# Kernel optimization log

Measured on AMD Instinct MI355X. Metric: run time of the kernel, lower is better.

Reference implementation:

```python
import jax, jax.numpy as jnp
import numpy as np

B, NQ, NK = 8, 1024, 1024
DQ = DK = DV = 512
H = 8
DH = DV // H
EPS = 1e-5
NEG = -1e9


def _layer_norm(x, g, b):
    mu = jnp.mean(x, axis=-1, keepdims=True)
    var = jnp.mean(jnp.square(x - mu), axis=-1, keepdims=True)
    return (x - mu) * jax.lax.rsqrt(var + EPS) * g + b


def setup_inputs() -> dict:
    key = jax.random.key(0)
    ks = jax.random.split(key, 16)
    s_q = 1.0 / np.sqrt(DQ)
    s_k = 1.0 / np.sqrt(DK)
    s_v = 1.0 / np.sqrt(DV)
    return {
        "Q": jax.random.normal(ks[0], (B, NQ, DQ), jnp.float32),
        "K": jax.random.normal(ks[1], (B, NK, DK), jnp.float32),
        "mask": jax.random.randint(ks[2], (B, NK), 0, 2, jnp.int32),
        "Wq": jax.random.uniform(ks[3], (DQ, DV), jnp.float32, -s_q, s_q),
        "bq": jax.random.uniform(ks[4], (DV,), jnp.float32, -s_q, s_q),
        "Wk": jax.random.uniform(ks[5], (DK, DV), jnp.float32, -s_k, s_k),
        "bk": jax.random.uniform(ks[6], (DV,), jnp.float32, -s_k, s_k),
        "Wv": jax.random.uniform(ks[7], (DK, DV), jnp.float32, -s_k, s_k),
        "bv": jax.random.uniform(ks[8], (DV,), jnp.float32, -s_k, s_k),
        "Wo": jax.random.uniform(ks[9], (DV, DV), jnp.float32, -s_v, s_v),
        "bo": jax.random.uniform(ks[10], (DV,), jnp.float32, -s_v, s_v),
        "g0": jnp.ones((DV,), jnp.float32),
        "b0": jnp.zeros((DV,), jnp.float32),
        "g1": jnp.ones((DV,), jnp.float32),
        "b1": jnp.zeros((DV,), jnp.float32),
    }


def reference(Q, K, mask, Wq, bq, Wk, bk, Wv, bv, Wo, bo, g0, b0, g1, b1):
    b = Q.shape[0]
    # projections: [B, N, DV] -> [B, N, H, DH]
    q = (Q @ Wq + bq).reshape(b, -1, H, DH)
    k = (K @ Wk + bk).reshape(b, -1, H, DH)
    v = (K @ Wv + bv).reshape(b, -1, H, DH)
    scores = jnp.einsum("bqhd,bkhd->bhqk", q, k) / np.sqrt(DH)  # [B,H,Nq,Nk]
    scores = jnp.where((mask == 0)[:, None, None, :], NEG, scores)
    A = jax.nn.softmax(scores, axis=-1)
    o = q + jnp.einsum("bhqk,bkhd->bqhd", A, v)  # residual on projected Q (per head)
    O = o.reshape(b, -1, DV)
    O = _layer_norm(O, g0, b0)
    O = O + jax.nn.relu(O @ Wo + bo)
    O = _layer_norm(O, g1, b1)
    return O
```

## Files before the change

kernel.cpp:

```cpp
#include <hip/hip_runtime.h>


typedef float f32x4 __attribute__((ext_vector_type(4)));
typedef short bf16x8 __attribute__((ext_vector_type(8)));
typedef unsigned short u16;

#define MFMA16 __builtin_amdgcn_mfma_f32_16x16x32_bf16

__device__ __forceinline__ float bf2f(u16 u){
    unsigned x = ((unsigned)u) << 16;
    return __builtin_bit_cast(float, x);
}
__device__ __forceinline__ u16 f2bf(float f){
    unsigned u = __builtin_bit_cast(unsigned, f);
    u = u + 0x7fffu + ((u >> 16) & 1u);
    return (u16)(u >> 16);
}

__global__ __launch_bounds__(256) void transpose_w(
    const float* __restrict__ Wq, const float* __restrict__ Wk,
    const float* __restrict__ Wv, const float* __restrict__ Wo,
    u16* __restrict__ wt)
{
    const int z = blockIdx.z;
    const float* W = (z == 0) ? Wq : (z == 1) ? Wk : (z == 2) ? Wv : Wo;
    u16* out = wt + (size_t)z * 512 * 512;

    __shared__ u16 tile[32][33];
    const int k0 = blockIdx.y * 32, n0 = blockIdx.x * 32;
    const int c = threadIdx.x & 31, r = threadIdx.x >> 5;
#pragma unroll
    for (int i = 0; i < 4; i++) {
        int rr = r + i * 8;
        tile[rr][c] = f2bf(W[(size_t)(k0 + rr) * 512 + n0 + c]);
    }
    __syncthreads();
#pragma unroll
    for (int i = 0; i < 4; i++) {
        int rr = r + i * 8;
        out[(size_t)(n0 + rr) * 512 + k0 + c] = tile[c][rr];
    }
}

__global__ __launch_bounds__(256) void transpose_v(
    const u16* __restrict__ vb, u16* __restrict__ vtg)
{
    __shared__ u16 tile[32][33];
    const int bh = blockIdx.z;
    const int b = bh >> 3, h = bh & 7;
    const int k0 = blockIdx.x * 32, d0 = blockIdx.y * 32;
    const int c = threadIdx.x & 31, r = threadIdx.x >> 5;
#pragma unroll
    for (int i = 0; i < 4; i++) {
        int rr = r + i * 8;
        tile[rr][c] = vb[(size_t)(b * 1024 + k0 + rr) * 512 + h * 64 + d0 + c];
    }
    __syncthreads();
#pragma unroll
    for (int i = 0; i < 4; i++) {
        int rr = r + i * 8;
        vtg[(size_t)(bh * 64 + d0 + rr) * 1024 + k0 + c] = tile[c][rr];
    }
}

__global__ __launch_bounds__(256) void gemm_proj(
    const float* __restrict__ Q, const float* __restrict__ K,
    const u16* __restrict__ wt,
    const float* __restrict__ bq, const float* __restrict__ bk, const float* __restrict__ bv,
    u16* __restrict__ qb, u16* __restrict__ kb, u16* __restrict__ vb)
{
    __shared__ __align__(16) u16 lds_a[128 * 40];
    __shared__ __align__(16) u16 lds_b[128 * 40];

    const int z = blockIdx.z;
    const float* X = (z == 0) ? Q : K;
    const u16* Wt = wt + (size_t)z * 512 * 512;
    const float* bias = (z == 0) ? bq : (z == 1) ? bk : bv;
    u16* outb = (z == 0) ? qb : (z == 1) ? kb : vb;

    const int bm = blockIdx.y, bn = blockIdx.x;
    const int t = threadIdx.x;
    const int wave = t >> 6, lane = t & 63, quad = lane >> 4, lm = lane & 15;
    const int wm = wave >> 1, wn = wave & 1;

    f32x4 acc[4][4];
    const f32x4 zz = {0.f, 0.f, 0.f, 0.f};
#pragma unroll
    for (int i = 0; i < 4; i++)
#pragma unroll
        for (int j = 0; j < 4; j++) acc[i][j] = zz;

    for (int k0 = 0; k0 < 512; k0 += 32) {
#pragma unroll
        for (int i = 0; i < 2; i++) {
            int idx = t + i * 256;
            int r = idx >> 2, c = (idx & 3) * 8;
            const float* xp = &X[(size_t)(bm * 128 + r) * 512 + k0 + c];
            f32x4 a0 = *(const f32x4*)xp;
            f32x4 a1 = *(const f32x4*)(xp + 4);
            bf16x8 xv;
#pragma unroll
            for (int j = 0; j < 4; j++) { xv[j] = (short)f2bf(a0[j]); xv[4 + j] = (short)f2bf(a1[j]); }
            *(bf16x8*)&lds_a[r * 40 + c] = xv;
            *(bf16x8*)&lds_b[r * 40 + c] =
                *(const bf16x8*)&Wt[(size_t)(bn * 128 + r) * 512 + k0 + c];
        }
        __syncthreads();
        bf16x8 af[4], bfr[4];
#pragma unroll
        for (int mi = 0; mi < 4; mi++)
            af[mi] = *(const bf16x8*)&lds_a[(wm * 64 + mi * 16 + lm) * 40 + quad * 8];
#pragma unroll
        for (int ni = 0; ni < 4; ni++)
            bfr[ni] = *(const bf16x8*)&lds_b[(wn * 64 + ni * 16 + lm) * 40 + quad * 8];
#pragma unroll
        for (int mi = 0; mi < 4; mi++)
#pragma unroll
            for (int ni = 0; ni < 4; ni++)
                acc[mi][ni] = MFMA16(af[mi], bfr[ni], acc[mi][ni], 0, 0, 0);
        __syncthreads();
    }

#pragma unroll
    for (int mi = 0; mi < 4; mi++) {
#pragma unroll
        for (int ni = 0; ni < 4; ni++) {
            const int col = bn * 128 + wn * 64 + ni * 16 + lm;
            const float bv_ = bias[col];
#pragma unroll
            for (int r = 0; r < 4; r++) {
                const int row = bm * 128 + wm * 64 + mi * 16 + quad * 4 + r;
                outb[(size_t)row * 512 + col] = f2bf(acc[mi][ni][r] + bv_);
            }
        }
    }
}

__global__ __launch_bounds__(256) void gemm_mlp(
    const u16* __restrict__ X, const u16* __restrict__ wt,
    const float* __restrict__ bo, const float* __restrict__ resid,
    float* __restrict__ outf)
{
    __shared__ __align__(16) u16 lds_a[128 * 40];
    __shared__ __align__(16) u16 lds_b[128 * 40];

    const u16* Wt = wt + (size_t)3 * 512 * 512;
    const int bm = blockIdx.y, bn = blockIdx.x;
    const int t = threadIdx.x;
    const int wave = t >> 6, lane = t & 63, quad = lane >> 4, lm = lane & 15;
    const int wm = wave >> 1, wn = wave & 1;

    f32x4 acc[4][4];
    const f32x4 zz = {0.f, 0.f, 0.f, 0.f};
#pragma unroll
    for (int i = 0; i < 4; i++)
#pragma unroll
        for (int j = 0; j < 4; j++) acc[i][j] = zz;

    for (int k0 = 0; k0 < 512; k0 += 32) {
#pragma unroll
        for (int i = 0; i < 2; i++) {
            int idx = t + i * 256;
            int r = idx >> 2, c = (idx & 3) * 8;
            *(bf16x8*)&lds_a[r * 40 + c] =
                *(const bf16x8*)&X[(size_t)(bm * 128 + r) * 512 + k0 + c];
            *(bf16x8*)&lds_b[r * 40 + c] =
                *(const bf16x8*)&Wt[(size_t)(bn * 128 + r) * 512 + k0 + c];
        }
        __syncthreads();
        bf16x8 af[4], bfr[4];
#pragma unroll
        for (int mi = 0; mi < 4; mi++)
            af[mi] = *(const bf16x8*)&lds_a[(wm * 64 + mi * 16 + lm) * 40 + quad * 8];
#pragma unroll
        for (int ni = 0; ni < 4; ni++)
            bfr[ni] = *(const bf16x8*)&lds_b[(wn * 64 + ni * 16 + lm) * 40 + quad * 8];
#pragma unroll
        for (int mi = 0; mi < 4; mi++)
#pragma unroll
            for (int ni = 0; ni < 4; ni++)
                acc[mi][ni] = MFMA16(af[mi], bfr[ni], acc[mi][ni], 0, 0, 0);
        __syncthreads();
    }

#pragma unroll
    for (int mi = 0; mi < 4; mi++) {
#pragma unroll
        for (int ni = 0; ni < 4; ni++) {
            const int col = bn * 128 + wn * 64 + ni * 16 + lm;
            const float bv_ = bo[col];
#pragma unroll
            for (int r = 0; r < 4; r++) {
                const int row = bm * 128 + wm * 64 + mi * 16 + quad * 4 + r;
                const size_t off = (size_t)row * 512 + col;
                outf[off] = resid[off] + fmaxf(acc[mi][ni][r] + bv_, 0.f);
            }
        }
    }
}

__global__ __launch_bounds__(256) void attn_kernel(
    const u16* __restrict__ qb, const u16* __restrict__ kb, const u16* __restrict__ vtg,
    const int* __restrict__ mask, float* __restrict__ O)
{
    __shared__ __align__(16) u16 k_tile[32 * 80];
    __shared__ __align__(16) u16 vt[64 * 40];
    __shared__ __align__(16) u16 p_st[4 * 16 * 40];
    __shared__ float mskf[1024];

    const int b = blockIdx.z, h = blockIdx.y, qt = blockIdx.x;
    const int t = threadIdx.x, wave = t >> 6, lane = t & 63;
    const int quad = lane >> 4, lm = lane & 15;
    const int q0 = qt * 64 + wave * 16;
    const size_t baseb = (size_t)b * 1024 * 512;
    const size_t vbase = (size_t)((b * 8 + h) * 64) * 1024;

#pragma unroll
    for (int i = 0; i < 4; i++) {
        int j = t + i * 256;
        mskf[j] = mask[b * 1024 + j] ? 1.0f : 0.0f;
    }

    bf16x8 aq[2];
#pragma unroll
    for (int s = 0; s < 2; s++)
        aq[s] = *(const bf16x8*)&qb[baseb + (size_t)(q0 + lm) * 512 + h * 64 + s * 32 + quad * 8];

    float lsum[4];
    f32x4 oacc[4];
    const f32x4 zz = {0.f, 0.f, 0.f, 0.f};
#pragma unroll
    for (int r = 0; r < 4; r++) lsum[r] = 0.f;
#pragma unroll
    for (int c = 0; c < 4; c++) oacc[c] = zz;

    const float SC2 = 0.125f * 1.44269504088896341f;
    const int key_t = t >> 3, dp = (t & 7) * 8;
    const int vd = t >> 2, vc = (t & 3) * 8;

    for (int kt = 0; kt < 32; ++kt) {
        const int keyg = kt * 32;
        *(bf16x8*)&k_tile[key_t * 80 + dp] =
            *(const bf16x8*)&kb[baseb + (size_t)(keyg + key_t) * 512 + h * 64 + dp];
        *(bf16x8*)&vt[vd * 40 + vc] =
            *(const bf16x8*)&vtg[vbase + (size_t)vd * 1024 + keyg + vc];
        __syncthreads();

        f32x4 S[2] = {zz, zz};
#pragma unroll
        for (int g = 0; g < 2; g++)
#pragma unroll
            for (int s = 0; s < 2; s++) {
                bf16x8 bk_ = *(const bf16x8*)&k_tile[(g * 16 + lm) * 80 + s * 32 + quad * 8];
                S[g] = MFMA16(aq[s], bk_, S[g], 0, 0, 0);
            }

#pragma unroll
        for (int g = 0; g < 2; g++) {
            const float mf = mskf[keyg + g * 16 + lm];
#pragma unroll
            for (int r = 0; r < 4; r++) {
                float p = __builtin_amdgcn_exp2f(S[g][r] * SC2) * mf;
                lsum[r] += p;
                p_st[wave * 640 + (quad * 4 + r) * 40 + g * 16 + lm] = f2bf(p);
            }
        }
        __syncthreads();

        bf16x8 ap = *(const bf16x8*)&p_st[wave * 640 + lm * 40 + quad * 8];
#pragma unroll
        for (int c = 0; c < 4; c++) {
            bf16x8 bv_ = *(const bf16x8*)&vt[(c * 16 + lm) * 40 + quad * 8];
            oacc[c] = MFMA16(ap, bv_, oacc[c], 0, 0, 0);
        }
        __syncthreads();
    }

#pragma unroll
    for (int r = 0; r < 4; r++) {
        float s = lsum[r];
        s += __shfl_xor(s, 1); s += __shfl_xor(s, 2);
        s += __shfl_xor(s, 4); s += __shfl_xor(s, 8);
        lsum[r] = s;
    }

#pragma unroll
    for (int c = 0; c < 4; c++) {
#pragma unroll
        for (int r = 0; r < 4; r++) {
            const int row = q0 + quad * 4 + r;
            const int d = h * 64 + c * 16 + lm;
            const size_t off = baseb + (size_t)row * 512 + d;
            O[off] = bf2f(qb[off]) + oacc[c][r] / lsum[r];
        }
    }
}

__global__ __launch_bounds__(256) void ln_kernel(
    const float* __restrict__ in, const float* __restrict__ g, const float* __restrict__ bsh,
    u16* __restrict__ outb, float* __restrict__ outf)
{
    const int row = blockIdx.x * 4 + (threadIdx.x >> 6);
    const int lane = threadIdx.x & 63;
    const float* x = in + (size_t)row * 512 + lane * 8;
    float v[8];
    *(f32x4*)&v[0] = *(const f32x4*)&x[0];
    *(f32x4*)&v[4] = *(const f32x4*)&x[4];
    float s = 0.f, sq = 0.f;
#pragma unroll
    for (int j = 0; j < 8; j++) { s += v[j]; sq += v[j] * v[j]; }
#pragma unroll
    for (int off = 1; off < 64; off <<= 1) {
        s += __shfl_xor(s, off);
        sq += __shfl_xor(sq, off);
    }
    const float mu = s * (1.f / 512.f);
    const float var = sq * (1.f / 512.f) - mu * mu;
    const float rs = rsqrtf(var + 1e-5f);
    float y[8];
#pragma unroll
    for (int j = 0; j < 8; j++) {
        int col = lane * 8 + j;
        y[j] = (v[j] - mu) * rs * g[col] + bsh[col];
    }
    if (outb != nullptr) {
        bf16x8 ov;
#pragma unroll
        for (int j = 0; j < 8; j++) ov[j] = (short)f2bf(y[j]);
        *(bf16x8*)&outb[(size_t)row * 512 + lane * 8] = ov;
    }
    if (outf != nullptr) {
        float* o = outf + (size_t)row * 512 + lane * 8;
        *(f32x4*)&o[0] = *(const f32x4*)&y[0];
        *(f32x4*)&o[4] = *(const f32x4*)&y[4];
    }
}

extern "C" void kernel_launch(void* const* d_in, const int* in_sizes, int n_in,
                              void* d_out, int out_size, void* d_ws, size_t ws_size,
                              hipStream_t stream) {
    const float* Q  = (const float*)d_in[0];
    const float* K  = (const float*)d_in[1];
    const int* mask = (const int*)d_in[2];
    const float* Wq = (const float*)d_in[3];
    const float* bq = (const float*)d_in[4];
    const float* Wk = (const float*)d_in[5];
    const float* bk = (const float*)d_in[6];
    const float* Wv = (const float*)d_in[7];
    const float* bv = (const float*)d_in[8];
    const float* Wo = (const float*)d_in[9];
    const float* bo = (const float*)d_in[10];
    const float* g0 = (const float*)d_in[11];
    const float* b0 = (const float*)d_in[12];
    const float* g1 = (const float*)d_in[13];
    const float* b1 = (const float*)d_in[14];
    float* out = (float*)d_out;

    char* ws = (char*)d_ws;
    const size_t MB = 1048576;
    u16*   wt  = (u16*)(ws);
    u16*   qb  = (u16*)(ws + 2 * MB);
    u16*   kb  = (u16*)(ws + 10 * MB);
    u16*   vtg = (u16*)(ws + 18 * MB);
    u16*   vb  = (u16*)(ws + 26 * MB);
    float* Of  = (float*)(ws + 26 * MB);
    u16*   O1b = (u16*)(ws + 2 * MB);
    float* O1f = (float*)(ws + 10 * MB);
    float* Uf  = (float*)(ws + 26 * MB);

    transpose_w<<<dim3(16, 16, 4), 256, 0, stream>>>(Wq, Wk, Wv, Wo, wt);
    gemm_proj<<<dim3(4, 64, 3), 256, 0, stream>>>(Q, K, wt, bq, bk, bv, qb, kb, vb);
    transpose_v<<<dim3(32, 2, 64), 256, 0, stream>>>(vb, vtg);
    attn_kernel<<<dim3(16, 8, 8), 256, 0, stream>>>(qb, kb, vtg, mask, Of);
    ln_kernel<<<2048, 256, 0, stream>>>(Of, g0, b0, O1b, O1f);
    gemm_mlp<<<dim3(4, 64, 1), 256, 0, stream>>>(O1b, wt, bo, O1f, Uf);
    ln_kernel<<<2048, 256, 0, stream>>>(Uf, g1, b1, nullptr, out);
}
```

Before: 214.5 us.

## Enlarge attention tiles to 128 queries by 64 keys and swizzle block order

The attention kernel now gives each wave 32 query rows instead of 16 and walks 64-key tiles instead of 32. This halves the number of K/V tile loads and barriers per query, and each K/V fragment read from shared memory is reused across two query sub-tiles. The grid becomes 1D, with an index remap that groups consecutive blocks over the same batch and heads so their K/V tiles can be shared through cache. In exchange it uses more registers and shared memory and launches fewer blocks (512 instead of 1024), which may lower occupancy.

```diff
diff --git a/kernel.cpp b/kernel.cpp
--- a/kernel.cpp
+++ b/kernel.cpp
@@ -203,97 +203,124 @@
     const u16* __restrict__ qb, const u16* __restrict__ kb, const u16* __restrict__ vtg,
     const int* __restrict__ mask, float* __restrict__ O)
 {
-    __shared__ __align__(16) u16 k_tile[32 * 80];
-    __shared__ __align__(16) u16 vt[64 * 40];
-    __shared__ __align__(16) u16 p_st[4 * 16 * 40];
+    __shared__ __align__(16) u16 k_tile[64 * 88];
+    __shared__ __align__(16) u16 vt[64 * 88];
+    __shared__ __align__(16) u16 p_st[4 * 32 * 88];
     __shared__ float mskf[1024];
 
-    const int b = blockIdx.z, h = blockIdx.y, qt = blockIdx.x;
+    const int i = blockIdx.x;
+    const int s_ = i >> 3;
+    const int bh = (i & 7) + 8 * (s_ >> 3);
+    const int qt = s_ & 7;
+    const int b = bh >> 3, h = bh & 7;
+
     const int t = threadIdx.x, wave = t >> 6, lane = t & 63;
     const int quad = lane >> 4, lm = lane & 15;
-    const int q0 = qt * 64 + wave * 16;
+    const int qbase = qt * 128 + wave * 32;
     const size_t baseb = (size_t)b * 1024 * 512;
     const size_t vbase = (size_t)((b * 8 + h) * 64) * 1024;
 
 #pragma unroll
-    for (int i = 0; i < 4; i++) {
-        int j = t + i * 256;
+    for (int ii = 0; ii < 4; ii++) {
+        int j = t + ii * 256;
         mskf[j] = mask[b * 1024 + j] ? 1.0f : 0.0f;
     }
 
-    bf16x8 aq[2];
-#pragma unroll
-    for (int s = 0; s < 2; s++)
-        aq[s] = *(const bf16x8*)&qb[baseb + (size_t)(q0 + lm) * 512 + h * 64 + s * 32 + quad * 8];
-
-    float lsum[4];
-    f32x4 oacc[4];
+    bf16x8 aq[2][2];
+#pragma unroll
+    for (int m = 0; m < 2; m++)
+#pragma unroll
+        for (int ks = 0; ks < 2; ks++)
+            aq[m][ks] = *(const bf16x8*)&qb[baseb +
+                (size_t)(qbase + m * 16 + lm) * 512 + h * 64 + ks * 32 + quad * 8];
+
+    float lsum[2][4];
+    f32x4 oacc[2][4];
     const f32x4 zz = {0.f, 0.f, 0.f, 0.f};
 #pragma unroll
-    for (int r = 0; r < 4; r++) lsum[r] = 0.f;
-#pragma unroll
-    for (int c = 0; c < 4; c++) oacc[c] = zz;
+    for (int m = 0; m < 2; m++) {
+#pragma unroll
+        for (int r = 0; r < 4; r++) lsum[m][r] = 0.f;
+#pragma unroll
+        for (int c = 0; c < 4; c++) oacc[m][c] = zz;
+    }
 
     const float SC2 = 0.125f * 1.44269504088896341f;
-    const int key_t = t >> 3, dp = (t & 7) * 8;
-    const int vd = t >> 2, vc = (t & 3) * 8;
-
-    for (int kt = 0; kt < 32; ++kt) {
-        const int keyg = kt * 32;
-        *(bf16x8*)&k_tile[key_t * 80 + dp] =
-            *(const bf16x8*)&kb[baseb + (size_t)(keyg + key_t) * 512 + h * 64 + dp];
-        *(bf16x8*)&vt[vd * 40 + vc] =
-            *(const bf16x8*)&vtg[vbase + (size_t)vd * 1024 + keyg + vc];
-        __syncthreads();
-
-        f32x4 S[2] = {zz, zz};
-#pragma unroll
-        for (int g = 0; g < 2; g++)
-#pragma unroll
-            for (int s = 0; s < 2; s++) {
-                bf16x8 bk_ = *(const bf16x8*)&k_tile[(g * 16 + lm) * 80 + s * 32 + quad * 8];
-                S[g] = MFMA16(aq[s], bk_, S[g], 0, 0, 0);
+    const int srow = t >> 2, scol = (t & 3) * 16;
+    u16* pw = &p_st[wave * 32 * 88];
+
+    for (int kt = 0; kt < 16; ++kt) {
+        const int keyg = kt * 64;
+        {
+            const u16* kp = &kb[baseb + (size_t)(keyg + srow) * 512 + h * 64 + scol];
+            *(bf16x8*)&k_tile[srow * 88 + scol]     = *(const bf16x8*)kp;
+            *(bf16x8*)&k_tile[srow * 88 + scol + 8] = *(const bf16x8*)(kp + 8);
+            const u16* vp = &vtg[vbase + (size_t)srow * 1024 + keyg + scol];
+            *(bf16x8*)&vt[srow * 88 + scol]     = *(const bf16x8*)vp;
+            *(bf16x8*)&vt[srow * 88 + scol + 8] = *(const bf16x8*)(vp + 8);
+        }
+        __syncthreads();
+
+        bf16x8 bk[4][2];
+#pragma unroll
+        for (int n = 0; n < 4; n++)
+#pragma unroll
+            for (int ks = 0; ks < 2; ks++)
+                bk[n][ks] = *(const bf16x8*)&k_tile[(n * 16 + lm) * 88 + ks * 32 + quad * 8];
+
+#pragma unroll
+        for (int m = 0; m < 2; m++) {
+#pragma unroll
+            for (int n = 0; n < 4; n++) {
+                f32x4 S = zz;
+                S = MFMA16(aq[m][0], bk[n][0], S, 0, 0, 0);
+                S = MFMA16(aq[m][1], bk[n][1], S, 0, 0, 0);
+                const float mf = mskf[keyg + n * 16 + lm];
+#pragma unroll
+                for (int r = 0; r < 4; r++) {
+                    float p = __builtin_amdgcn_exp2f(S[r] * SC2) * mf;
+                    lsum[m][r] += p;
+                    pw[(m * 16 + quad * 4 + r) * 88 + n * 16 + lm] = f2bf(p);
+                }
             }
-
-#pragma unroll
-        for (int g = 0; g < 2; g++) {
-            const float mf = mskf[keyg + g * 16 + lm];
+        }
+
+#pragma unroll
+        for (int m = 0; m < 2; m++) {
+#pragma unroll
+            for (int ks = 0; ks < 2; ks++) {
+                bf16x8 ap = *(const bf16x8*)&pw[(m * 16 + lm) * 88 + ks * 32 + quad * 8];
+#pragma unroll
+                for (int c = 0; c < 4; c++) {
+                    bf16x8 bv_ = *(const bf16x8*)&vt[(c * 16 + lm) * 88 + ks * 32 + quad * 8];
+                    oacc[m][c] = MFMA16(ap, bv_, oacc[m][c], 0, 0, 0);
+                }
+            }
+        }
+        __syncthreads();
+    }
+
+#pragma unroll
+    for (int m = 0; m < 2; m++)
+#pragma unroll
+        for (int r = 0; r < 4; r++) {
+            float s = lsum[m][r];
+            s += __shfl_xor(s, 1); s += __shfl_xor(s, 2);
+            s += __shfl_xor(s, 4); s += __shfl_xor(s, 8);
+            lsum[m][r] = s;
+        }
+
+#pragma unroll
+    for (int m = 0; m < 2; m++)
+#pragma unroll
+        for (int c = 0; c < 4; c++)
 #pragma unroll
             for (int r = 0; r < 4; r++) {
-                float p = __builtin_amdgcn_exp2f(S[g][r] * SC2) * mf;
-                lsum[r] += p;
-                p_st[wave * 640 + (quad * 4 + r) * 40 + g * 16 + lm] = f2bf(p);
+                const int row = qbase + m * 16 + quad * 4 + r;
+                const int d = h * 64 + c * 16 + lm;
+                const size_t off = baseb + (size_t)row * 512 + d;
+                O[off] = bf2f(qb[off]) + oacc[m][c][r] / lsum[m][r];
             }
-        }
-        __syncthreads();
-
-        bf16x8 ap = *(const bf16x8*)&p_st[wave * 640 + lm * 40 + quad * 8];
-#pragma unroll
-        for (int c = 0; c < 4; c++) {
-            bf16x8 bv_ = *(const bf16x8*)&vt[(c * 16 + lm) * 40 + quad * 8];
-            oacc[c] = MFMA16(ap, bv_, oacc[c], 0, 0, 0);
-        }
-        __syncthreads();
-    }
-
-#pragma unroll
-    for (int r = 0; r < 4; r++) {
-        float s = lsum[r];
-        s += __shfl_xor(s, 1); s += __shfl_xor(s, 2);
-        s += __shfl_xor(s, 4); s += __shfl_xor(s, 8);
-        lsum[r] = s;
-    }
-
-#pragma unroll
-    for (int c = 0; c < 4; c++) {
-#pragma unroll
-        for (int r = 0; r < 4; r++) {
-            const int row = q0 + quad * 4 + r;
-            const int d = h * 64 + c * 16 + lm;
-            const size_t off = baseb + (size_t)row * 512 + d;
-            O[off] = bf2f(qb[off]) + oacc[c][r] / lsum[r];
-        }
-    }
 }
 
 __global__ __launch_bounds__(256) void ln_kernel(
@@ -371,7 +398,7 @@
     transpose_w<<<dim3(16, 16, 4), 256, 0, stream>>>(Wq, Wk, Wv, Wo, wt);
     gemm_proj<<<dim3(4, 64, 3), 256, 0, stream>>>(Q, K, wt, bq, bk, bv, qb, kb, vb);
     transpose_v<<<dim3(32, 2, 64), 256, 0, stream>>>(vb, vtg);
-    attn_kernel<<<dim3(16, 8, 8), 256, 0, stream>>>(qb, kb, vtg, mask, Of);
+    attn_kernel<<<512, 256, 0, stream>>>(qb, kb, vtg, mask, Of);
     ln_kernel<<<2048, 256, 0, stream>>>(Of, g0, b0, O1b, O1f);
     gemm_mlp<<<dim3(4, 64, 1), 256, 0, stream>>>(O1b, wt, bo, O1f, Uf);
     ln_kernel<<<2048, 256, 0, stream>>>(Uf, g1, b1, nullptr, out);
```

Result: faster. 208.5 us (-2.8%).
